# Kernel tuning notes

Hardware: AMD Instinct MI355X
Metric: run time of the kernel (lower is better)

Reference implementation:

```python
import jax, jax.numpy as jnp
import numpy as np

EPSILON = 10.0
N_ITERS = 10
TOL = 1e-06
N, DIM = 8192, 128


def setup_inputs() -> dict:
    key = jax.random.key(0)
    kx, ky = jax.random.split(key)
    x = jax.random.normal(kx, (N, DIM), dtype=jnp.float32)
    y = jax.random.normal(ky, (N, DIM), dtype=jnp.float32)
    return {"x": x, "y": y}


def _sinkhorn_plan(C):
    # uniform marginals, as in the torch module defaults
    n = C.shape[0]
    a = jnp.full((n,), 1.0 / n, dtype=C.dtype)
    b = a
    K = jnp.exp(-C / EPSILON)  # [n, n]
    u0 = jnp.ones((n,), dtype=C.dtype)
    v0 = jnp.ones((n,), dtype=C.dtype)

    def step(carry, _):
        u, v, done = carry
        u_new = a / (K @ v)
        v_new = b / (K.T @ u_new)
        # torch breaks AFTER applying the update, so the converging step is kept
        conv = jnp.linalg.norm(u_new - u) < TOL
        u = jnp.where(done, u, u_new)
        v = jnp.where(done, v, v_new)
        return (u, v, done | conv), None

    (u, v, _), _ = jax.lax.scan(step, (u0, v0, jnp.array(False)), None, length=N_ITERS)
    # diag(u) @ K @ diag(v) == u[:,None] * K * v[None,:] (no diag materialization)
    return u[:, None] * K * v[None, :]


def reference(x, y):
    # torch.cdist(x, y, p=2): pairwise L2 distances [n, n]
    x2 = jnp.sum(x * x, axis=1)
    y2 = jnp.sum(y * y, axis=1)
    d2 = x2[:, None] + y2[None, :] - 2.0 * (x @ y.T)
    C = jnp.sqrt(jnp.maximum(d2, 0.0))

    P = _sinkhorn_plan(C)
    transport_cost = jnp.sum(P * C)
    entropy = -jnp.sum(P * jnp.log(P + 1e-09))
    divergence = transport_cost + EPSILON * entropy
    return divergence, P
```

## Files before the change

### kernel.cpp

```cpp
#include <hip/hip_runtime.h>

#define N 8192
#define DIM 128
#define EPS 10.0f
#define AINV (1.0f / 8192.0f)
#define C1 (-0.14426950408889634f)
#define C1SQ (0.020813712f)

typedef __attribute__((ext_vector_type(8))) short short8;
typedef __attribute__((ext_vector_type(4))) float f32x4;

static __device__ __forceinline__ unsigned short f2bf(float f) {
  unsigned int b = __float_as_uint(f);
  unsigned int lsb = (b >> 16) & 1u;
  b += 0x7fffu + lsb;
  return (unsigned short)(b >> 16);
}

__global__ __launch_bounds__(256) void k_convert(const float* __restrict__ x, const float* __restrict__ y,
                                                 unsigned short* __restrict__ xb, unsigned short* __restrict__ yb,
                                                 float* __restrict__ x2, float* __restrict__ y2,
                                                 float* __restrict__ u, float* __restrict__ vpartB,
                                                 double* __restrict__ accs) {
  int r = blockIdx.x * 4 + (threadIdx.x >> 6);
  int l = threadIdx.x & 63;
  const float* src = (r < N) ? (x + (size_t)r * DIM) : (y + (size_t)(r - N) * DIM);
  float2 f = ((const float2*)src)[l];
  unsigned short* dstbase = (r < N) ? xb : yb;
  int rr = (r < N) ? r : r - N;
  ushort2 h; h.x = f2bf(f.x); h.y = f2bf(f.y);
  int idx2 = ((rr >> 4) << 10) + ((l >> 2) << 6) + ((rr & 15) << 2) + (l & 3);
  ((ushort2*)dstbase)[idx2] = h;
  float s = f.x * f.x + f.y * f.y;
#pragma unroll
  for (int off = 32; off >= 1; off >>= 1) s += __shfl_down(s, off);
  if (l == 0) { if (r < N) x2[r] = s; else y2[r - N] = s; }
  if (r < N) {
    if (l == 0) { u[r] = 1.f; vpartB[r] = AINV; }
    else if (l < 16) vpartB[(size_t)l * N + r] = 0.f;
  }
  if (r == 0 && l == 0) { accs[0] = 0.0; accs[1] = 0.0; }
}

__global__ __launch_bounds__(256, 3) void k_pass(const unsigned short* __restrict__ Ab,
                                                 const unsigned short* __restrict__ Bb,
                                                 const float* __restrict__ a2, const float* __restrict__ b2,
                                                 const float* __restrict__ wpart,
                                                 float* __restrict__ outpart,
                                                 float* __restrict__ u_arr,
                                                 int write_u) {
  __shared__ float wv_lds[1024];
  __shared__ float b2_lds[1024];
  const int jc = blockIdx.x;
  const int ic = blockIdx.y;
  const int i0 = ic * 128;
  const int tid = threadIdx.x;
  const int wid = tid >> 6, lane = tid & 63;
  const int wr = (wid >> 1) * 64, wc = (wid & 1) * 32;
  const int lhi = lane >> 4, llo = lane & 15;
  const uint4* afrag = (const uint4*)Ab;
  const uint4* bfrag = (const uint4*)Bb;
  short8 afr[4][4];
#pragma unroll
  for (int kk = 0; kk < 4; ++kk)
#pragma unroll
    for (int m = 0; m < 4; ++m)
      afr[kk][m] = *(const short8*)(afrag + ((ic * 8 + (wid >> 1) * 4 + m) * 256 + kk * 64 + lane));
  float a2v[4][4], rsum[4][4];
#pragma unroll
  for (int m = 0; m < 4; ++m)
#pragma unroll
    for (int r = 0; r < 4; ++r) {
      a2v[m][r] = a2[i0 + wr + m * 16 + lhi * 4 + r] * C1SQ;
      rsum[m][r] = 0.f;
    }
  {
    const float4* wp4 = (const float4*)wpart;
    int w4 = jc * 256 + tid;
    float4 s4 = wp4[w4];
#pragma unroll
    for (int q = 1; q < 16; ++q) {
      float4 p = wp4[(size_t)q * 2048 + w4];
      s4.x += p.x; s4.y += p.y; s4.z += p.z; s4.w += p.w;
    }
    float4 wn;
    wn.x = AINV * __builtin_amdgcn_rcpf(s4.x);
    wn.y = AINV * __builtin_amdgcn_rcpf(s4.y);
    wn.z = AINV * __builtin_amdgcn_rcpf(s4.z);
    wn.w = AINV * __builtin_amdgcn_rcpf(s4.w);
    ((float4*)wv_lds)[tid] = wn;
    float4 b4 = ((const float4*)b2)[w4];
    b4.x *= C1SQ; b4.y *= C1SQ; b4.z *= C1SQ; b4.w *= C1SQ;
    ((float4*)b2_lds)[tid] = b4;
    if (write_u && ic == 0) ((float4*)u_arr)[w4] = wn;
  }
  __syncthreads();
  for (int sc = 0; sc < 16; ++sc) {
    float wv[2], b2v[2];
#pragma unroll
    for (int n = 0; n < 2; ++n) {
      int jl = sc * 64 + wc + n * 16 + llo;
      wv[n] = wv_lds[jl];
      b2v[n] = b2_lds[jl];
    }
    f32x4 acc[4][2];
    f32x4 zero = {0.f, 0.f, 0.f, 0.f};
#pragma unroll
    for (int m = 0; m < 4; ++m)
#pragma unroll
      for (int n = 0; n < 2; ++n) acc[m][n] = zero;
#pragma unroll
    for (int kk = 0; kk < 4; ++kk) {
      short8 bfr[2];
#pragma unroll
      for (int n = 0; n < 2; ++n)
        bfr[n] = *(const short8*)(bfrag + ((jc * 64 + sc * 4 + (wid & 1) * 2 + n) * 256 + kk * 64 + lane));
#pragma unroll
      for (int m = 0; m < 4; ++m)
#pragma unroll
        for (int n = 0; n < 2; ++n)
          acc[m][n] = __builtin_amdgcn_mfma_f32_16x16x32_bf16(afr[kk][m], bfr[n], acc[m][n], 0, 0, 0);
    }
#pragma unroll
    for (int m = 0; m < 4; ++m)
#pragma unroll
      for (int n = 0; n < 2; ++n)
#pragma unroll
        for (int r = 0; r < 4; ++r) {
          float tt = fmaf(-2.f * C1SQ, acc[m][n][r], a2v[m][r] + b2v[n]);
          float ss = __builtin_amdgcn_sqrtf(fmaxf(tt, 0.f));
          rsum[m][r] = fmaf(__builtin_amdgcn_exp2f(-ss), wv[n], rsum[m][r]);
        }
  }
#pragma unroll
  for (int m = 0; m < 4; ++m)
#pragma unroll
    for (int r = 0; r < 4; ++r) {
      float s = rsum[m][r];
      s += __shfl_xor(s, 1);
      s += __shfl_xor(s, 2);
      s += __shfl_xor(s, 4);
      s += __shfl_xor(s, 8);
      rsum[m][r] = s;
    }
  if (llo == 0) {
    float* vp = outpart + (size_t)(jc * 2 + (wid & 1)) * N;
#pragma unroll
    for (int m = 0; m < 4; ++m)
#pragma unroll
      for (int r = 0; r < 4; ++r)
        vp[i0 + wr + m * 16 + lhi * 4 + r] = rsum[m][r];
  }
}

__global__ void k_vrecon(const float* __restrict__ vpartB, const float* __restrict__ y2,
                         float2* __restrict__ vy2) {
  int j = blockIdx.x * 256 + threadIdx.x;
  float s = 0.f;
#pragma unroll
  for (int q = 0; q < 16; ++q) s += vpartB[(size_t)q * N + j];
  float2 o; o.x = AINV * __builtin_amdgcn_rcpf(s); o.y = y2[j];
  vy2[j] = o;
}

__global__ __launch_bounds__(256) void k_final(const unsigned short* __restrict__ xb,
                                               const unsigned short* __restrict__ yb,
                                               const float* __restrict__ x2,
                                               const float* __restrict__ u, const float2* __restrict__ vy2,
                                               float* __restrict__ D, double* __restrict__ accs) {
  __shared__ double r0[256], r1[256];
  const int b = blockIdx.x;
  const int i0 = (b >> 1) * 16;
  const int ch = (b & 1) * 4096;
  const int tid = threadIdx.x;
  const int wid = tid >> 6, lane = tid & 63;
  const int lhi = lane >> 4, llo = lane & 15;
  const int wc = wid * 32;
  const uint4* xfrag = (const uint4*)xb;
  const uint4* yfrag = (const uint4*)yb;
  short8 af[4];
#pragma unroll
  for (int kk = 0; kk < 4; ++kk)
    af[kk] = *(const short8*)(xfrag + ((b >> 1) * 256 + kk * 64 + lane));
  float x2v[4], uvv[4];
#pragma unroll
  for (int r = 0; r < 4; ++r) {
    int i = i0 + lhi * 4 + r;
    x2v[r] = x2[i];
    uvv[r] = u[i];
  }
  float lc = 0.f, le = 0.f;
  for (int sc = 0; sc < 32; ++sc) {
    const int c0 = ch + sc * 128 + wc;
    float2 vy[2];
#pragma unroll
    for (int n = 0; n < 2; ++n) vy[n] = vy2[c0 + n * 16 + llo];
    f32x4 acc[2];
    f32x4 zero = {0.f, 0.f, 0.f, 0.f};
    acc[0] = zero; acc[1] = zero;
#pragma unroll
    for (int kk = 0; kk < 4; ++kk) {
      short8 bfr[2];
#pragma unroll
      for (int n = 0; n < 2; ++n)
        bfr[n] = *(const short8*)(yfrag + (((c0 + n * 16) >> 4) * 256 + kk * 64 + lane));
#pragma unroll
      for (int n = 0; n < 2; ++n)
        acc[n] = __builtin_amdgcn_mfma_f32_16x16x32_bf16(af[kk], bfr[n], acc[n], 0, 0, 0);
    }
#pragma unroll
    for (int n = 0; n < 2; ++n)
#pragma unroll
      for (int r = 0; r < 4; ++r) {
        float d2 = fmaf(-2.f, acc[n][r], x2v[r] + vy[n].y);
        float c = __builtin_amdgcn_sqrtf(fmaxf(d2, 0.f));
        float k = __builtin_amdgcn_exp2f(c * C1);
        float p = uvv[r] * k * vy[n].x;
        D[1 + (size_t)(i0 + lhi * 4 + r) * N + c0 + n * 16 + llo] = p;
        lc = fmaf(p, c, lc);
        le = fmaf(p, __logf(p + 1e-9f), le);
      }
  }
  r0[tid] = (double)lc;
  r1[tid] = (double)le;
  __syncthreads();
  for (int s = 128; s > 0; s >>= 1) {
    if (tid < s) {
      r0[tid] += r0[tid + s];
      r1[tid] += r1[tid + s];
    }
    __syncthreads();
  }
  if (tid == 0) {
    atomicAdd(&accs[0], r0[0]);
    atomicAdd(&accs[1], r1[0]);
  }
}

__global__ void k_write_div(float* D, const double* accs) {
  if (threadIdx.x == 0 && blockIdx.x == 0)
    D[0] = (float)(accs[0] - (double)EPS * accs[1]);
}

extern "C" void kernel_launch(void* const* d_in, const int* in_sizes, int n_in,
                              void* d_out, int out_size, void* d_ws, size_t ws_size,
                              hipStream_t stream) {
  const float* x = (const float*)d_in[0];
  const float* y = (const float*)d_in[1];
  float* D = (float*)d_out;
  char* w = (char*)d_ws;
  unsigned short* xb = (unsigned short*)w;
  unsigned short* yb = (unsigned short*)(w + 2097152);
  float* fb = (float*)(w + 4194304);
  float* x2 = fb;
  float* y2 = fb + 8192;
  float* u = fb + 16384;
  float* vpartA = fb + 24576;
  float* vpartB = vpartA + 16 * N;
  float2* vy2 = (float2*)(vpartB + 16 * N);
  double* accs = (double*)(vy2 + N);

  k_convert<<<4096, 256, 0, stream>>>(x, y, xb, yb, x2, y2, u, vpartB, accs);
  k_pass<<<dim3(8, 64), 256, 0, stream>>>(xb, yb, x2, y2, vpartB, vpartA, u, 0);
  k_pass<<<dim3(8, 64), 256, 0, stream>>>(yb, xb, y2, x2, vpartA, vpartB, u, 0);
  k_pass<<<dim3(8, 64), 256, 0, stream>>>(xb, yb, x2, y2, vpartB, vpartA, u, 0);
  k_pass<<<dim3(8, 64), 256, 0, stream>>>(yb, xb, y2, x2, vpartA, vpartB, u, 1);
  k_vrecon<<<32, 256, 0, stream>>>(vpartB, y2, vy2);
  k_final<<<1024, 256, 0, stream>>>(xb, yb, x2, u, vy2, D, accs);
  k_write_div<<<1, 64, 0, stream>>>(D, accs);
}
```

Measured before the change: 225.8 us.

## Halve per-block row tiles in Sinkhorn passes and split final kernel finer

Each pass block now handles 64 rows instead of 128, with twice as many blocks and a higher occupancy hint. The two LDS arrays are merged into one interleaved float2 array. The final kernel splits each row strip into four column chunks instead of two, doubling block count. It also swaps __logf for the hardware log2 and applies ln2 at the end. The aim is more parallelism and latency hiding, at the cost of reloading the B fragments more often and issuing more atomics.

```diff
diff --git a/kernel.cpp b/kernel.cpp
--- a/kernel.cpp
+++ b/kernel.cpp
@@ -6,6 +6,7 @@
 #define AINV (1.0f / 8192.0f)
 #define C1 (-0.14426950408889634f)
 #define C1SQ (0.020813712f)
+#define LN2 (0.6931471805599453)
 
 typedef __attribute__((ext_vector_type(8))) short short8;
 typedef __attribute__((ext_vector_type(4))) float f32x4;
@@ -42,36 +43,34 @@
   if (r == 0 && l == 0) { accs[0] = 0.0; accs[1] = 0.0; }
 }
 
-__global__ __launch_bounds__(256, 3) void k_pass(const unsigned short* __restrict__ Ab,
+__global__ __launch_bounds__(256, 4) void k_pass(const unsigned short* __restrict__ Ab,
                                                  const unsigned short* __restrict__ Bb,
                                                  const float* __restrict__ a2, const float* __restrict__ b2,
                                                  const float* __restrict__ wpart,
                                                  float* __restrict__ outpart,
                                                  float* __restrict__ u_arr,
                                                  int write_u) {
-  __shared__ float wv_lds[1024];
-  __shared__ float b2_lds[1024];
+  __shared__ float2 wb_lds[1024];
   const int jc = blockIdx.x;
   const int ic = blockIdx.y;
-  const int i0 = ic * 128;
+  const int i0 = ic * 64;
   const int tid = threadIdx.x;
   const int wid = tid >> 6, lane = tid & 63;
-  const int wr = (wid >> 1) * 64, wc = (wid & 1) * 32;
   const int lhi = lane >> 4, llo = lane & 15;
   const uint4* afrag = (const uint4*)Ab;
   const uint4* bfrag = (const uint4*)Bb;
-  short8 afr[4][4];
+  short8 afr[4][2];
 #pragma unroll
   for (int kk = 0; kk < 4; ++kk)
 #pragma unroll
-    for (int m = 0; m < 4; ++m)
-      afr[kk][m] = *(const short8*)(afrag + ((ic * 8 + (wid >> 1) * 4 + m) * 256 + kk * 64 + lane));
-  float a2v[4][4], rsum[4][4];
-#pragma unroll
-  for (int m = 0; m < 4; ++m)
+    for (int m = 0; m < 2; ++m)
+      afr[kk][m] = *(const short8*)(afrag + ((ic * 4 + (wid >> 1) * 2 + m) * 256 + kk * 64 + lane));
+  float a2v[2][4], rsum[2][4];
+#pragma unroll
+  for (int m = 0; m < 2; ++m)
 #pragma unroll
     for (int r = 0; r < 4; ++r) {
-      a2v[m][r] = a2[i0 + wr + m * 16 + lhi * 4 + r] * C1SQ;
+      a2v[m][r] = a2[i0 + (wid >> 1) * 32 + m * 16 + lhi * 4 + r] * C1SQ;
       rsum[m][r] = 0.f;
     }
   {
@@ -88,25 +87,23 @@
     wn.y = AINV * __builtin_amdgcn_rcpf(s4.y);
     wn.z = AINV * __builtin_amdgcn_rcpf(s4.z);
     wn.w = AINV * __builtin_amdgcn_rcpf(s4.w);
-    ((float4*)wv_lds)[tid] = wn;
     float4 b4 = ((const float4*)b2)[w4];
-    b4.x *= C1SQ; b4.y *= C1SQ; b4.z *= C1SQ; b4.w *= C1SQ;
-    ((float4*)b2_lds)[tid] = b4;
+    wb_lds[tid * 4 + 0] = make_float2(wn.x, b4.x * C1SQ);
+    wb_lds[tid * 4 + 1] = make_float2(wn.y, b4.y * C1SQ);
+    wb_lds[tid * 4 + 2] = make_float2(wn.z, b4.z * C1SQ);
+    wb_lds[tid * 4 + 3] = make_float2(wn.w, b4.w * C1SQ);
     if (write_u && ic == 0) ((float4*)u_arr)[w4] = wn;
   }
   __syncthreads();
   for (int sc = 0; sc < 16; ++sc) {
-    float wv[2], b2v[2];
-#pragma unroll
-    for (int n = 0; n < 2; ++n) {
-      int jl = sc * 64 + wc + n * 16 + llo;
-      wv[n] = wv_lds[jl];
-      b2v[n] = b2_lds[jl];
-    }
-    f32x4 acc[4][2];
+    float2 wb[2];
+#pragma unroll
+    for (int n = 0; n < 2; ++n)
+      wb[n] = wb_lds[sc * 64 + (wid & 1) * 32 + n * 16 + llo];
+    f32x4 acc[2][2];
     f32x4 zero = {0.f, 0.f, 0.f, 0.f};
 #pragma unroll
-    for (int m = 0; m < 4; ++m)
+    for (int m = 0; m < 2; ++m)
 #pragma unroll
       for (int n = 0; n < 2; ++n) acc[m][n] = zero;
 #pragma unroll
@@ -116,24 +113,24 @@
       for (int n = 0; n < 2; ++n)
         bfr[n] = *(const short8*)(bfrag + ((jc * 64 + sc * 4 + (wid & 1) * 2 + n) * 256 + kk * 64 + lane));
 #pragma unroll
-      for (int m = 0; m < 4; ++m)
+      for (int m = 0; m < 2; ++m)
 #pragma unroll
         for (int n = 0; n < 2; ++n)
           acc[m][n] = __builtin_amdgcn_mfma_f32_16x16x32_bf16(afr[kk][m], bfr[n], acc[m][n], 0, 0, 0);
     }
 #pragma unroll
-    for (int m = 0; m < 4; ++m)
+    for (int m = 0; m < 2; ++m)
 #pragma unroll
       for (int n = 0; n < 2; ++n)
 #pragma unroll
         for (int r = 0; r < 4; ++r) {
-          float tt = fmaf(-2.f * C1SQ, acc[m][n][r], a2v[m][r] + b2v[n]);
+          float tt = fmaf(-2.f * C1SQ, acc[m][n][r], a2v[m][r] + wb[n].y);
           float ss = __builtin_amdgcn_sqrtf(fmaxf(tt, 0.f));
-          rsum[m][r] = fmaf(__builtin_amdgcn_exp2f(-ss), wv[n], rsum[m][r]);
+          rsum[m][r] = fmaf(__builtin_amdgcn_exp2f(-ss), wb[n].x, rsum[m][r]);
         }
   }
 #pragma unroll
-  for (int m = 0; m < 4; ++m)
+  for (int m = 0; m < 2; ++m)
 #pragma unroll
     for (int r = 0; r < 4; ++r) {
       float s = rsum[m][r];
@@ -146,10 +143,10 @@
   if (llo == 0) {
     float* vp = outpart + (size_t)(jc * 2 + (wid & 1)) * N;
 #pragma unroll
-    for (int m = 0; m < 4; ++m)
+    for (int m = 0; m < 2; ++m)
 #pragma unroll
       for (int r = 0; r < 4; ++r)
-        vp[i0 + wr + m * 16 + lhi * 4 + r] = rsum[m][r];
+        vp[i0 + (wid >> 1) * 32 + m * 16 + lhi * 4 + r] = rsum[m][r];
   }
 }
 
@@ -170,8 +167,8 @@
                                                float* __restrict__ D, double* __restrict__ accs) {
   __shared__ double r0[256], r1[256];
   const int b = blockIdx.x;
-  const int i0 = (b >> 1) * 16;
-  const int ch = (b & 1) * 4096;
+  const int i0 = (b >> 2) * 16;
+  const int ch = (b & 3) * 2048;
   const int tid = threadIdx.x;
   const int wid = tid >> 6, lane = tid & 63;
   const int lhi = lane >> 4, llo = lane & 15;
@@ -181,7 +178,7 @@
   short8 af[4];
 #pragma unroll
   for (int kk = 0; kk < 4; ++kk)
-    af[kk] = *(const short8*)(xfrag + ((b >> 1) * 256 + kk * 64 + lane));
+    af[kk] = *(const short8*)(xfrag + ((b >> 2) * 256 + kk * 64 + lane));
   float x2v[4], uvv[4];
 #pragma unroll
   for (int r = 0; r < 4; ++r) {
@@ -190,7 +187,7 @@
     uvv[r] = u[i];
   }
   float lc = 0.f, le = 0.f;
-  for (int sc = 0; sc < 32; ++sc) {
+  for (int sc = 0; sc < 16; ++sc) {
     const int c0 = ch + sc * 128 + wc;
     float2 vy[2];
 #pragma unroll
@@ -218,7 +215,7 @@
         float p = uvv[r] * k * vy[n].x;
         D[1 + (size_t)(i0 + lhi * 4 + r) * N + c0 + n * 16 + llo] = p;
         lc = fmaf(p, c, lc);
-        le = fmaf(p, __logf(p + 1e-9f), le);
+        le = fmaf(p, __builtin_amdgcn_logf(p + 1e-9f), le);
       }
   }
   r0[tid] = (double)lc;
@@ -239,7 +236,7 @@
 
 __global__ void k_write_div(float* D, const double* accs) {
   if (threadIdx.x == 0 && blockIdx.x == 0)
-    D[0] = (float)(accs[0] - (double)EPS * accs[1]);
+    D[0] = (float)(accs[0] - (double)EPS * (LN2 * accs[1]));
 }
 
 extern "C" void kernel_launch(void* const* d_in, const int* in_sizes, int n_in,
@@ -261,11 +258,11 @@
   double* accs = (double*)(vy2 + N);
 
   k_convert<<<4096, 256, 0, stream>>>(x, y, xb, yb, x2, y2, u, vpartB, accs);
-  k_pass<<<dim3(8, 64), 256, 0, stream>>>(xb, yb, x2, y2, vpartB, vpartA, u, 0);
-  k_pass<<<dim3(8, 64), 256, 0, stream>>>(yb, xb, y2, x2, vpartA, vpartB, u, 0);
-  k_pass<<<dim3(8, 64), 256, 0, stream>>>(xb, yb, x2, y2, vpartB, vpartA, u, 0);
-  k_pass<<<dim3(8, 64), 256, 0, stream>>>(yb, xb, y2, x2, vpartA, vpartB, u, 1);
+  k_pass<<<dim3(8, 128), 256, 0, stream>>>(xb, yb, x2, y2, vpartB, vpartA, u, 0);
+  k_pass<<<dim3(8, 128), 256, 0, stream>>>(yb, xb, y2, x2, vpartA, vpartB, u, 0);
+  k_pass<<<dim3(8, 128), 256, 0, stream>>>(xb, yb, x2, y2, vpartB, vpartA, u, 0);
+  k_pass<<<dim3(8, 128), 256, 0, stream>>>(yb, xb, y2, x2, vpartA, vpartB, u, 1);
   k_vrecon<<<32, 256, 0, stream>>>(vpartB, y2, vy2);
-  k_final<<<1024, 256, 0, stream>>>(xb, yb, x2, u, vy2, D, accs);
+  k_final<<<2048, 256, 0, stream>>>(xb, yb, x2, u, vy2, D, accs);
   k_write_div<<<1, 64, 0, stream>>>(D, accs);
 }
```

Result: faster. 216.2 us, median of 2 (-4.2%).
